# Kernel optimization log

Hardware: AMD Instinct MI355X
Metric: run time of the kernel (lower is better)

## Reference

```python
import jax, jax.numpy as jnp
import numpy as np

EMBED_DIM = 1024
EXPAND_RATIO = 128  # head_dim; n_heads = EMBED_DIM // EXPAND_RATIO = 8
B, N = 4, 2048


def setup_inputs() -> dict:
    key = jax.random.key(0)
    ks = jax.random.split(key, 6)
    std = 0.02
    d = EMBED_DIM
    return {
        "x": jax.random.normal(ks[0], (B, N, d), dtype=jnp.float32),
        "Wq": jax.random.normal(ks[1], (d, d), dtype=jnp.float32) * std,
        "Wk": jax.random.normal(ks[2], (d, d), dtype=jnp.float32) * std,
        "Wv": jax.random.normal(ks[3], (d, d), dtype=jnp.float32) * std,
        "Wo": jax.random.normal(ks[4], (d, d), dtype=jnp.float32) * std,
        "norm_w": jnp.ones((d,), dtype=jnp.float32),
    }


def _rmsnorm(x, w, eps=1e-6):
    return x * jax.lax.rsqrt(jnp.mean(x * x, axis=-1, keepdims=True) + eps) * w


def _gla_scan(q, k, v, g):
    # q,k,v,g: [b, n, h, d]; state S: [b, h, d_k, d_v]
    b, n, h, d = q.shape
    qs, ks_, vs, gs = (jnp.moveaxis(t, 1, 0) for t in (q, k, v, g))  # [n,b,h,d]
    S0 = jnp.zeros((b, h, d, d), dtype=q.dtype)

    def step(S, inp):
        q_t, k_t, v_t, g_t = inp
        # S_t = diag(exp(g_t)) S_{t-1} + k_t^T v_t (gate on key dim)
        S = jnp.exp(g_t)[..., :, None] * S + k_t[..., :, None] * v_t[..., None, :]
        o_t = jnp.einsum('bhk,bhkv->bhv', q_t, S)
        return S, o_t

    _, outs = jax.lax.scan(step, S0, (qs, ks_, vs, gs))
    return jnp.moveaxis(outs, 0, 1)  # [b, n, h, d]


def reference(x, Wq, Wk, Wv, Wo, norm_w):
    b, n, D = x.shape
    hd = EXPAND_RATIO
    h = D // hd

    q = jax.nn.silu(x @ Wq.T)          # q_activation = silu
    f = jax.nn.sigmoid(x @ Wk.T)       # f = sigmoid(k_proj(x))
    log_f = jax.nn.log_sigmoid(f)      # faithful: logsigmoid applied to f (lower_bound=None path)
    k = 1.0 - f
    v = x @ Wv.T

    def split_heads(t):
        return t.reshape(b, n, h, hd)

    out = _gla_scan(split_heads(q), split_heads(k), split_heads(v), split_heads(log_f))
    out = out.reshape(b, n, D)
    out = _rmsnorm(out, norm_w)        # norm_pos='ogate', no output gate
    return out @ Wo.T
```

## Files before the change

### kernel.cpp

```cpp
#include <hip/hip_runtime.h>
#include <cstdint>
#include <cstddef>


typedef unsigned short u16;
using f32x4  = __attribute__((ext_vector_type(4))) float;
using bf16x8 = __attribute__((ext_vector_type(8))) short;

__device__ __forceinline__ float bf2f(u16 u) {
  union { unsigned int i; float f; } v; v.i = ((unsigned int)u) << 16; return v.f;
}
__device__ __forceinline__ u16 f2bf(float f) {
  union { float f; unsigned int i; } v; v.f = f;
  unsigned int r = v.i + 0x7fffu + ((v.i >> 16) & 1u);
  return (u16)(r >> 16);
}
__device__ __forceinline__ void async_load16(const void* g, void* l) {
  __builtin_amdgcn_global_load_lds(
      (const __attribute__((address_space(1))) unsigned int*)(uintptr_t)g,
      (__attribute__((address_space(3))) unsigned int*)(uintptr_t)l, 16, 0, 0);
}

__device__ __forceinline__ void gemm128_core(const u16* __restrict__ Ag, const u16* __restrict__ Bg,
                                             u16* smem, f32x4 (&acc)[4][4]) {
  const int tid = threadIdx.x;
  const int lane = tid & 63, wave = tid >> 6;
  const int wm = (wave & 1) * 64, wn = (wave >> 1) * 64;
  const int r = lane & 15, quad = lane >> 4;
  const int xk = r & 7;
  const u16* baseA0 = smem + (wm + r) * 64 + ((quad ^ xk) & 7) * 8;
  const u16* baseA1 = smem + (wm + r) * 64 + (((quad + 4) ^ xk) & 7) * 8;
  const u16* baseB0 = smem + 8192 + (wn + r) * 64 + ((quad ^ xk) & 7) * 8;
  const u16* baseB1 = smem + 8192 + (wn + r) * 64 + (((quad + 4) ^ xk) & 7) * 8;
  const int soff = (tid >> 3) * 1024 + (((tid & 7) ^ ((tid >> 3) & 7)) * 8);
  u16* dA = smem + wave * 512;
  u16* dB = smem + 8192 + wave * 512;
  for (int kt = 0; kt < 16; ++kt) {
    __syncthreads();
    const u16* As = Ag + kt * 64 + soff;
    const u16* Bs = Bg + kt * 64 + soff;
#pragma unroll
    for (int it = 0; it < 4; ++it) {
      async_load16(As + it * 32768, dA + it * 2048);
      async_load16(Bs + it * 32768, dB + it * 2048);
    }
    __syncthreads();
    bf16x8 af[4], bv[4];
#pragma unroll
    for (int i = 0; i < 4; ++i) af[i] = *(const bf16x8*)(baseA0 + i * 1024);
#pragma unroll
    for (int j = 0; j < 4; ++j) bv[j] = *(const bf16x8*)(baseB0 + j * 1024);
#pragma unroll
    for (int i = 0; i < 4; ++i)
#pragma unroll
      for (int j = 0; j < 4; ++j)
        acc[i][j] = __builtin_amdgcn_mfma_f32_16x16x32_bf16(af[i], bv[j], acc[i][j], 0, 0, 0);
#pragma unroll
    for (int i = 0; i < 4; ++i) af[i] = *(const bf16x8*)(baseA1 + i * 1024);
#pragma unroll
    for (int j = 0; j < 4; ++j) bv[j] = *(const bf16x8*)(baseB1 + j * 1024);
#pragma unroll
    for (int i = 0; i < 4; ++i)
#pragma unroll
      for (int j = 0; j < 4; ++j)
        acc[i][j] = __builtin_amdgcn_mfma_f32_16x16x32_bf16(af[i], bv[j], acc[i][j], 0, 0, 0);
  }
}

__global__ __launch_bounds__(256) void cast_f32_bf16(const float* __restrict__ src,
                                                     u16* __restrict__ dst, int n4) {
  int i = blockIdx.x * 256 + threadIdx.x;
  if (i >= n4) return;
  float4 v = ((const float4*)src)[i];
  unsigned int lo = (unsigned)f2bf(v.x) | ((unsigned)f2bf(v.y) << 16);
  unsigned int hi = (unsigned)f2bf(v.z) | ((unsigned)f2bf(v.w) << 16);
  ((uint2*)dst)[i] = make_uint2(lo, hi);
}

__global__ __launch_bounds__(256) void cast_w4(const float* __restrict__ w0, const float* __restrict__ w1,
                                               const float* __restrict__ w2, const float* __restrict__ w3,
                                               u16* __restrict__ d0, u16* __restrict__ d1,
                                               u16* __restrict__ d2, u16* __restrict__ d3) {
  const float* src = blockIdx.y == 0 ? w0 : (blockIdx.y == 1 ? w1 : (blockIdx.y == 2 ? w2 : w3));
  u16* dst = blockIdx.y == 0 ? d0 : (blockIdx.y == 1 ? d1 : (blockIdx.y == 2 ? d2 : d3));
  int i = blockIdx.x * 256 + threadIdx.x;
  float4 v = ((const float4*)src)[i];
  unsigned int lo = (unsigned)f2bf(v.x) | ((unsigned)f2bf(v.y) << 16);
  unsigned int hi = (unsigned)f2bf(v.z) | ((unsigned)f2bf(v.w) << 16);
  ((uint2*)dst)[i] = make_uint2(lo, hi);
}

__global__ __launch_bounds__(256) void hgru_gemm_qkv(
    const u16* __restrict__ Xb, const u16* __restrict__ Wqb, const u16* __restrict__ Wkb,
    const u16* __restrict__ Wvb, u16* __restrict__ Qb, u16* __restrict__ Kb,
    u16* __restrict__ Vb) {
  __shared__ alignas(16) u16 smem[16384];
  const int which = blockIdx.y >> 3, bn = blockIdx.y & 7;
  const u16* W = which == 0 ? Wqb : (which == 1 ? Wkb : Wvb);
  const u16* Ag = Xb + (size_t)blockIdx.x * 128 * 1024;
  const u16* Bg = W + (size_t)bn * 128 * 1024;
  f32x4 acc[4][4] = {};
  gemm128_core(Ag, Bg, smem, acc);
  const int tid = threadIdx.x, lane = tid & 63, wave = tid >> 6;
  const int wm = (wave & 1) * 64, wn = (wave >> 1) * 64;
  const int r = lane & 15, quad = lane >> 4;
#pragma unroll
  for (int i = 0; i < 4; ++i)
#pragma unroll
    for (int j = 0; j < 4; ++j)
#pragma unroll
      for (int reg = 0; reg < 4; ++reg) {
        int m = blockIdx.x * 128 + wm + i * 16 + quad * 4 + reg;
        int n = bn * 128 + wn + j * 16 + r;
        size_t off = (size_t)m * 1024 + n;
        float z = acc[i][j][reg];
        if (which == 0) {
          Qb[off] = f2bf(z / (1.f + __expf(-z)));
        } else if (which == 1) {
          float ek = __expf(-z);
          Kb[off] = f2bf(ek / (1.f + ek));
        } else {
          Vb[off] = f2bf(z);
        }
      }
}

__global__ __launch_bounds__(256) void hgru_scan(
    const u16* __restrict__ Qg, const u16* __restrict__ Kg, const u16* __restrict__ Vg,
    u16* __restrict__ O) {
  __shared__ alignas(16) char smem[59008];
  float* sb = (float*)(smem);
  u16* sU   = (u16*)(smem + 16512);
  u16* sKt  = (u16*)(smem + 33920);
  u16* sVt1 = (u16*)(smem + 44160);
  u16* sQ   = (u16*)(smem + 33920);
  u16* sK   = (u16*)(smem + 42624);
  u16* sAm  = (u16*)(smem + 51328);
  u16* sVt2 = (u16*)(smem + 53888);

  const int tid = threadIdx.x, blk = blockIdx.x;
  const int vh = blk & 1, c = (blk >> 1) & 63, bh = blk >> 7, h = bh & 7, bb_ = bh >> 3;
  const size_t rb = (size_t)(bb_ * 2048 + c * 32) * 1024 + h * 128;
  const bool haveP = (c > 0);
  const size_t rb1 = haveP ? rb - 32 * 1024 : rb;

  const int lane = tid & 63, wave = tid >> 6;
  const int r = lane & 15, quad = lane >> 4;
  const int ts = tid & 31;
  const int g8 = tid >> 5;

  uint4 Q2[2], K2[2], K1[2], V2, V1;
#pragma unroll
  for (int it = 0; it < 2; ++it) {
    Q2[it] = *(const uint4*)(Qg + rb  + (size_t)ts * 1024 + (it * 8 + g8) * 8);
    K2[it] = *(const uint4*)(Kg + rb  + (size_t)ts * 1024 + (it * 8 + g8) * 8);
    K1[it] = *(const uint4*)(Kg + rb1 + (size_t)ts * 1024 + (it * 8 + g8) * 8);
  }
  V2 = *(const uint4*)(Vg + rb  + (size_t)ts * 1024 + vh * 64 + g8 * 8);
  V1 = *(const uint4*)(Vg + rb1 + (size_t)ts * 1024 + vh * 64 + g8 * 8);

  f32x4 accU[2][4] = {};
  const int vm = (wave & 1) * 32, in = (wave >> 1) * 64;

  if (haveP) {
    { const int col = tid & 127, half = tid >> 7;
      float run = 0.f;
      const size_t gb = rb1 + (size_t)(half * 16) * 1024 + col;
#pragma unroll
      for (int t = 0; t < 16; ++t) {
        float kv = bf2f(Kg[gb + (size_t)t * 1024]);
        run -= __logf(1.f + __expf(-(1.f - kv)));
        sb[(half * 16 + t) * 129 + col] = run;
      } }
    __syncthreads();
    { if (tid >> 7) { const int col = tid & 127; float fix = sb[15 * 129 + col];
#pragma unroll
        for (int t = 16; t < 32; ++t) sb[t * 129 + col] += fix; } }
    __syncthreads();
#pragma unroll
    for (int it = 0; it < 2; ++it) {
      const int i8 = it * 8 + g8;
      const u16* kp = (const u16*)&K1[it];
#pragma unroll
      for (int e = 0; e < 8; ++e) {
        int i = i8 * 8 + e;
        float bs = sb[ts * 129 + i];
        float bC = sb[31 * 129 + i];
        sKt[i * 40 + ts] = f2bf(bf2f(kp[e]) * __expf(bC - bs));
      }
    }
    { const u16* vp = (const u16*)&V1;
#pragma unroll
      for (int e = 0; e < 8; ++e) sVt1[(g8 * 8 + e) * 40 + ts] = vp[e]; }
    __syncthreads();
#pragma unroll
    for (int mi = 0; mi < 2; ++mi) {
      bf16x8 af = *(const bf16x8*)(sVt1 + (vm + mi * 16 + r) * 40 + quad * 8);
#pragma unroll
      for (int nj = 0; nj < 4; ++nj) {
        bf16x8 bv = *(const bf16x8*)(sKt + (in + nj * 16 + r) * 40 + quad * 8);
        accU[mi][nj] = __builtin_amdgcn_mfma_f32_16x16x32_bf16(af, bv, accU[mi][nj], 0, 0, 0);
      }
    }
  }
  { const int col = tid & 127, half = tid >> 7;
    float run = 0.f;
    const size_t gb = rb + (size_t)(half * 16) * 1024 + col;
#pragma unroll
    for (int t = 0; t < 16; ++t) {
      float kv = bf2f(Kg[gb + (size_t)t * 1024]);
      run -= __logf(1.f + __expf(-(1.f - kv)));
      sb[(half * 16 + t) * 129 + col] = run;
    } }
  __syncthreads();
  { if (tid >> 7) { const int col = tid & 127; float fix = sb[15 * 129 + col];
#pragma unroll
      for (int t = 16; t < 32; ++t) sb[t * 129 + col] += fix; } }
  if (haveP) {
#pragma unroll
    for (int mi = 0; mi < 2; ++mi)
#pragma unroll
      for (int nj = 0; nj < 4; ++nj)
#pragma unroll
        for (int reg = 0; reg < 4; ++reg) {
          int vl = vm + mi * 16 + quad * 4 + reg;
          int i  = in + nj * 16 + r;
          sU[vl * 136 + i] = f2bf(accU[mi][nj][reg]);
        }
  }
  __syncthreads();
#pragma unroll
  for (int it = 0; it < 2; ++it) {
    const int i8 = it * 8 + g8;
    const u16* qp = (const u16*)&Q2[it];
    const u16* kp = (const u16*)&K2[it];
    u16 qo[8], ko[8];
#pragma unroll
    for (int e = 0; e < 8; ++e) {
      int i = i8 * 8 + e;
      float bt = sb[ts * 129 + i];
      qo[e] = f2bf(bf2f(qp[e]) * __expf(bt));
      ko[e] = f2bf(bf2f(kp[e]) * __expf(-bt));
    }
    *(uint4*)(sQ + ts * 136 + i8 * 8) = *(const uint4*)qo;
    *(uint4*)(sK + ts * 136 + i8 * 8) = *(const uint4*)ko;
  }
  { const u16* vp = (const u16*)&V2;
#pragma unroll
    for (int e = 0; e < 8; ++e) sVt2[(g8 * 8 + e) * 40 + ts] = vp[e]; }
  __syncthreads();
  { const int mi = wave & 1, nj = wave >> 1;
    f32x4 a1 = {0.f, 0.f, 0.f, 0.f};
#pragma unroll
    for (int ks = 0; ks < 4; ++ks) {
      bf16x8 af = *(const bf16x8*)(sQ + (mi * 16 + r) * 136 + ks * 32 + quad * 8);
      bf16x8 bk = *(const bf16x8*)(sK + (nj * 16 + r) * 136 + ks * 32 + quad * 8);
      a1 = __builtin_amdgcn_mfma_f32_16x16x32_bf16(af, bk, a1, 0, 0, 0);
    }
#pragma unroll
    for (int reg = 0; reg < 4; ++reg) {
      int t = mi * 16 + quad * 4 + reg, s = nj * 16 + r;
      sAm[t * 40 + s] = (s <= t) ? f2bf(a1[reg]) : (u16)0;
    } }
  __syncthreads();
  { const int mi = wave & 1, no = (wave >> 1) * 32;
    bf16x8 af0 = *(const bf16x8*)(sAm + (mi * 16 + r) * 40 + quad * 8);
    bf16x8 afq[4];
    if (haveP) {
#pragma unroll
      for (int ks = 0; ks < 4; ++ks)
        afq[ks] = *(const bf16x8*)(sQ + (mi * 16 + r) * 136 + ks * 32 + quad * 8);
    }
#pragma unroll
    for (int j = 0; j < 2; ++j) {
      f32x4 acc2 = {0.f, 0.f, 0.f, 0.f};
      bf16x8 bv0 = *(const bf16x8*)(sVt2 + (no + j * 16 + r) * 40 + quad * 8);
      acc2 = __builtin_amdgcn_mfma_f32_16x16x32_bf16(af0, bv0, acc2, 0, 0, 0);
      if (haveP) {
#pragma unroll
        for (int ks = 0; ks < 4; ++ks) {
          bf16x8 bs = *(const bf16x8*)(sU + (no + j * 16 + r) * 136 + ks * 32 + quad * 8);
          acc2 = __builtin_amdgcn_mfma_f32_16x16x32_bf16(afq[ks], bs, acc2, 0, 0, 0);
        }
      }
#pragma unroll
      for (int reg = 0; reg < 4; ++reg) {
        int t = mi * 16 + quad * 4 + reg;
        int vg = vh * 64 + no + j * 16 + r;
        O[rb + (size_t)t * 1024 + vg] = f2bf(acc2[reg]);
      }
    } }
}

__global__ __launch_bounds__(256) void hgru_rmsnorm(const u16* __restrict__ O,
                                                    const float* __restrict__ w,
                                                    u16* __restrict__ On) {
  __shared__ float sred[4];
  const int row = blockIdx.x, tid = threadIdx.x;
  const size_t base = (size_t)row * 1024;
  float vals[4];
  float ss = 0.f;
#pragma unroll
  for (int k = 0; k < 4; ++k) {
    float v = bf2f(O[base + k * 256 + tid]);
    vals[k] = v;
    ss += v * v;
  }
#pragma unroll
  for (int m = 32; m >= 1; m >>= 1) ss += __shfl_xor(ss, m);
  if ((tid & 63) == 0) sred[tid >> 6] = ss;
  __syncthreads();
  float tot = sred[0] + sred[1] + sred[2] + sred[3];
  float scale = rsqrtf(tot * (1.f / 1024.f) + 1e-6f);
#pragma unroll
  for (int k = 0; k < 4; ++k)
    On[base + k * 256 + tid] = f2bf(vals[k] * scale * w[k * 256 + tid]);
}

__global__ __launch_bounds__(256) void hgru_gemm_out(const u16* __restrict__ Ab,
                                                     const u16* __restrict__ Wob,
                                                     float* __restrict__ out) {
  __shared__ alignas(16) u16 smem[16384];
  const u16* Ag = Ab + (size_t)blockIdx.x * 128 * 1024;
  const u16* Bg = Wob + (size_t)blockIdx.y * 128 * 1024;
  f32x4 acc[4][4] = {};
  gemm128_core(Ag, Bg, smem, acc);
  const int tid = threadIdx.x, lane = tid & 63, wave = tid >> 6;
  const int wm = (wave & 1) * 64, wn = (wave >> 1) * 64;
  const int r = lane & 15, quad = lane >> 4;
#pragma unroll
  for (int i = 0; i < 4; ++i)
#pragma unroll
    for (int j = 0; j < 4; ++j)
#pragma unroll
      for (int reg = 0; reg < 4; ++reg) {
        int m = blockIdx.x * 128 + wm + i * 16 + quad * 4 + reg;
        int n = blockIdx.y * 128 + wn + j * 16 + r;
        out[(size_t)m * 1024 + n] = acc[i][j][reg];
      }
}

extern "C" void kernel_launch(void* const* d_in, const int* in_sizes, int n_in,
                              void* d_out, int out_size, void* d_ws, size_t ws_size,
                              hipStream_t stream) {
  const float* x  = (const float*)d_in[0];
  const float* Wq = (const float*)d_in[1];
  const float* Wk = (const float*)d_in[2];
  const float* Wv = (const float*)d_in[3];
  const float* Wo = (const float*)d_in[4];
  const float* nw = (const float*)d_in[5];
  float* out = (float*)d_out;
  char* ws = (char*)d_ws;

  u16* Xb   = (u16*)(ws + 0);
  u16* Wqb  = (u16*)(ws + 16777216);
  u16* Wkb  = (u16*)(ws + 18874368);
  u16* Wvb  = (u16*)(ws + 20971520);
  u16* Wob  = (u16*)(ws + 23068672);
  u16* Qb   = (u16*)(ws + 25165824);
  u16* Kb   = (u16*)(ws + 41943040);
  u16* Vb   = (u16*)(ws + 58720256);
  u16* Obf  = (u16*)(ws + 75497472);
  u16* On   = Xb;

  cast_f32_bf16<<<8192, 256, 0, stream>>>(x, Xb, 2097152);
  dim3 gw(1024, 4);
  cast_w4<<<gw, 256, 0, stream>>>(Wq, Wk, Wv, Wo, Wqb, Wkb, Wvb, Wob);

  dim3 gq(64, 24);
  hgru_gemm_qkv<<<gq, 256, 0, stream>>>(Xb, Wqb, Wkb, Wvb, Qb, Kb, Vb);
  hgru_scan<<<4096, 256, 0, stream>>>(Qb, Kb, Vb, Obf);
  hgru_rmsnorm<<<8192, 256, 0, stream>>>(Obf, nw, On);
  dim3 go(64, 8);
  hgru_gemm_out<<<go, 256, 0, stream>>>(On, Wob, out);
}
```

Baseline: 263.1 us.

## Double-buffer GEMM K-tiles with async prefetch of the next tile

The bf16 MFMA GEMM core moves from a single-buffered 64-wide K tile, with two barriers per step, to a double-buffered 32-wide K tile. The next tile's global-to-LDS async loads are issued right after one barrier, so they overlap the MFMAs on the current buffer. The LDS swizzle and addressing are reworked for the narrower tile while the total LDS footprint stays the same. The trade-off is twice as many loop iterations and barriers, and less MFMA work per step to hide load latency.

```diff
diff --git a/kernel.cpp b/kernel.cpp
--- a/kernel.cpp
+++ b/kernel.cpp
@@ -27,38 +27,36 @@
   const int lane = tid & 63, wave = tid >> 6;
   const int wm = (wave & 1) * 64, wn = (wave >> 1) * 64;
   const int r = lane & 15, quad = lane >> 4;
-  const int xk = r & 7;
-  const u16* baseA0 = smem + (wm + r) * 64 + ((quad ^ xk) & 7) * 8;
-  const u16* baseA1 = smem + (wm + r) * 64 + (((quad + 4) ^ xk) & 7) * 8;
-  const u16* baseB0 = smem + 8192 + (wn + r) * 64 + ((quad ^ xk) & 7) * 8;
-  const u16* baseB1 = smem + 8192 + (wn + r) * 64 + (((quad + 4) ^ xk) & 7) * 8;
-  const int soff = (tid >> 3) * 1024 + (((tid & 7) ^ ((tid >> 3) & 7)) * 8);
+  const int xk = r & 3;
+  const u16* baseA = smem + (wm + r) * 32 + ((quad ^ xk) & 3) * 8;
+  const u16* baseB = smem + 4096 + (wn + r) * 32 + ((quad ^ xk) & 3) * 8;
+  const int soff = (tid >> 2) * 1024 + (((tid & 3) ^ ((tid >> 2) & 3)) * 8);
   u16* dA = smem + wave * 512;
-  u16* dB = smem + 8192 + wave * 512;
-  for (int kt = 0; kt < 16; ++kt) {
+  u16* dB = smem + 4096 + wave * 512;
+#pragma unroll
+  for (int it = 0; it < 2; ++it) {
+    async_load16(Ag + it * 65536 + soff, dA + it * 2048);
+    async_load16(Bg + it * 65536 + soff, dB + it * 2048);
+  }
+#pragma unroll 2
+  for (int kt = 0; kt < 32; ++kt) {
+    const int cb = (kt & 1) * 8192;
     __syncthreads();
-    const u16* As = Ag + kt * 64 + soff;
-    const u16* Bs = Bg + kt * 64 + soff;
-#pragma unroll
-    for (int it = 0; it < 4; ++it) {
-      async_load16(As + it * 32768, dA + it * 2048);
-      async_load16(Bs + it * 32768, dB + it * 2048);
-    }
-    __syncthreads();
+    if (kt < 31) {
+      const int nb = ((kt + 1) & 1) * 8192;
+      const u16* As = Ag + (kt + 1) * 32 + soff;
+      const u16* Bs = Bg + (kt + 1) * 32 + soff;
+#pragma unroll
+      for (int it = 0; it < 2; ++it) {
+        async_load16(As + it * 65536, dA + nb + it * 2048);
+        async_load16(Bs + it * 65536, dB + nb + it * 2048);
+      }
+    }
     bf16x8 af[4], bv[4];
 #pragma unroll
-    for (int i = 0; i < 4; ++i) af[i] = *(const bf16x8*)(baseA0 + i * 1024);
-#pragma unroll
-    for (int j = 0; j < 4; ++j) bv[j] = *(const bf16x8*)(baseB0 + j * 1024);
-#pragma unroll
-    for (int i = 0; i < 4; ++i)
-#pragma unroll
-      for (int j = 0; j < 4; ++j)
-        acc[i][j] = __builtin_amdgcn_mfma_f32_16x16x32_bf16(af[i], bv[j], acc[i][j], 0, 0, 0);
-#pragma unroll
-    for (int i = 0; i < 4; ++i) af[i] = *(const bf16x8*)(baseA1 + i * 1024);
-#pragma unroll
-    for (int j = 0; j < 4; ++j) bv[j] = *(const bf16x8*)(baseB1 + j * 1024);
+    for (int i = 0; i < 4; ++i) af[i] = *(const bf16x8*)(baseA + cb + i * 512);
+#pragma unroll
+    for (int j = 0; j < 4; ++j) bv[j] = *(const bf16x8*)(baseB + cb + j * 512);
 #pragma unroll
     for (int i = 0; i < 4; ++i)
 #pragma unroll
```

After: 255.8 us. -2.8%, faster.
